# Performance work log

Hardware: AMD Instinct MI355X
Metric: run time of the kernel (lower is better)

The kernel has to match this reference:

```python
import jax, jax.numpy as jnp
import numpy as np

N = 50000
E = 200000
IN = 165
HID = 100
H1, H2, H3 = 8, 8, 1
NC = 2
DIM1 = HID * H1  # 800
DIM2 = HID * H2  # 800
NEG_SLOPE = 0.2


def setup_inputs() -> dict:
    key = jax.random.key(0)
    ks = jax.random.split(key, 20)
    p = lambda k, shape: jax.random.normal(k, shape, jnp.float32) * 0.05
    x = jax.random.normal(ks[0], (N, IN), jnp.float32)
    edge_index = jax.random.randint(ks[1], (2, E), 0, N, jnp.int64)
    return {
        "x": x,
        "edge_index": edge_index,
        "W1": p(ks[2], (IN, H1 * HID)), "a1s": p(ks[3], (H1, HID)),
        "a1d": p(ks[4], (H1, HID)), "b1": jnp.zeros((H1 * HID,), jnp.float32),
        "W2": p(ks[5], (DIM1, H2 * HID)), "a2s": p(ks[6], (H2, HID)),
        "a2d": p(ks[7], (H2, HID)), "b2": jnp.zeros((H2 * HID,), jnp.float32),
        # gat3: 800 -> 2, 1 head, mean (concat=False)
        "W3": p(ks[8], (DIM2, H3 * NC)), "a3s": p(ks[9], (H3, NC)),
        "a3d": p(ks[10], (H3, NC)), "b3": jnp.zeros((NC,), jnp.float32),
        # residual / skip linears (bias=False), stored [in, out]
        "Wres1": p(ks[11], (DIM1, DIM2)),
        "Wres2": p(ks[12], (DIM2, NC)),
        "Wskip": p(ks[13], (IN, NC)),
    }


def gat_conv(x, W, a_src, a_dst, b, src, dst, n, heads, ch, concat):
    # h: [n, heads, ch] projected node features
    h = (x @ W).reshape(n, heads, ch)
    e_src = (h * a_src).sum(-1)  # [n, heads]
    e_dst = (h * a_dst).sum(-1)
    # per-edge attention logits, LeakyReLU as in PyG GATConv
    e = jax.nn.leaky_relu(e_src[src] + e_dst[dst], NEG_SLOPE)  # [Etot, heads]
    # segment softmax over incoming edges of each destination node
    m = jax.ops.segment_max(e, dst, num_segments=n)
    ex = jnp.exp(e - m[dst])
    denom = jax.ops.segment_sum(ex, dst, num_segments=n)
    alpha = ex / (denom[dst] + 1e-16)
    # weighted scatter-aggregation of source messages
    out = jax.ops.segment_sum(alpha[:, :, None] * h[src], dst, num_segments=n)
    out = out.reshape(n, heads * ch) if concat else out.mean(axis=1)
    return out + b


def reference(x, edge_index, W1, a1s, a1d, b1, W2, a2s, a2d, b2,
              W3, a3s, a3d, b3, Wres1, Wres2, Wskip):
    n = x.shape[0]
    loop = jnp.arange(n, dtype=edge_index.dtype)  # PyG adds self-loops by default
    src = jnp.concatenate([edge_index[0], loop])
    dst = jnp.concatenate([edge_index[1], loop])

    h1 = jax.nn.elu(gat_conv(x, W1, a1s, a1d, b1, src, dst, n, H1, HID, True))
    h2 = gat_conv(h1, W2, a2s, a2d, b2, src, dst, n, H2, HID, True) + h1 @ Wres1
    h2 = jax.nn.elu(h2)
    logits = gat_conv(h2, W3, a3s, a3d, b3, src, dst, n, H3, NC, False)
    logits = logits + h2 @ Wres2 + x @ Wskip
    return logits
```

## Files before the change

kernel.cpp:

```cpp
#include <hip/hip_runtime.h>

#define NN     50000
#define NE     200000
#define ETOT   250000
#define FIN    165
#define KP1    192
#define HEADS  8
#define CH     100
#define DIM    800
#define MPAD   50048
#define NP1    896
#define DIM2   1600
#define NP2    1664
#define NEG    0.2f
#define CHK    64

typedef unsigned short u16;
typedef unsigned int   u32;
typedef __bf16 bf16x8 __attribute__((ext_vector_type(8)));
typedef float  f32x4  __attribute__((ext_vector_type(4)));

__device__ __forceinline__ u16 f2b(float f) {
  u32 u = __float_as_uint(f);
  u = (u + 0x7FFFu + ((u >> 16) & 1u)) >> 16;
  return (u16)u;
}
__device__ __forceinline__ float b2f(u16 u) { return __uint_as_float(((u32)u) << 16); }

__global__ void k_count(const int* __restrict__ ei, int* __restrict__ cnt) {
  int e = blockIdx.x * 256 + threadIdx.x;
  if (e >= ETOT) return;
  int d = (e < NE) ? ei[NE + e] : (e - NE);
  atomicAdd(&cnt[d], 1);
}
__global__ void k_bsum(const int* __restrict__ cnt, int* __restrict__ bs) {
  __shared__ int sm[256];
  int i = blockIdx.x * 256 + threadIdx.x;
  sm[threadIdx.x] = (i < NN) ? cnt[i] : 0;
  __syncthreads();
  for (int off = 128; off; off >>= 1) {
    if (threadIdx.x < off) sm[threadIdx.x] += sm[threadIdx.x + off];
    __syncthreads();
  }
  if (!threadIdx.x) bs[blockIdx.x] = sm[0];
}
__global__ void k_top(int* __restrict__ bs, int* __restrict__ rs, int nb) {
  __shared__ int sm[256];
  int t = threadIdx.x;
  int v = (t < nb) ? bs[t] : 0;
  sm[t] = v; __syncthreads();
  for (int off = 1; off < 256; off <<= 1) {
    int add = (t >= off) ? sm[t - off] : 0;
    __syncthreads();
    sm[t] += add;
    __syncthreads();
  }
  if (t < nb) bs[t] = sm[t] - v;
  if (!t) rs[NN] = ETOT;
}
__global__ void k_scan(const int* __restrict__ cnt, const int* __restrict__ bs, int* __restrict__ rs) {
  __shared__ int sm[256];
  int t = threadIdx.x, i = blockIdx.x * 256 + t;
  int v = (i < NN) ? cnt[i] : 0;
  sm[t] = v; __syncthreads();
  for (int off = 1; off < 256; off <<= 1) {
    int add = (t >= off) ? sm[t - off] : 0;
    __syncthreads();
    sm[t] += add;
    __syncthreads();
  }
  if (i < NN) rs[i] = bs[blockIdx.x] + sm[t] - v;
}
__global__ void k_fill(const int* __restrict__ ei, const int* __restrict__ rs,
                       int* __restrict__ cur, int* __restrict__ esrc) {
  int e = blockIdx.x * 256 + threadIdx.x;
  if (e >= ETOT) return;
  int s, d;
  if (e < NE) { s = ei[e]; d = ei[NE + e]; } else { s = d = e - NE; }
  int pos = atomicAdd(&cur[d], 1);
  esrc[rs[d] + pos] = s;
}

__global__ void k_cvt_x(const float* __restrict__ x, u16* __restrict__ A) {
  int idx = blockIdx.x * 256 + threadIdx.x;
  int r = idx / KP1, k = idx - r * KP1;
  float v = (r < NN && k < FIN) ? x[r * FIN + k] : 0.f;
  A[idx] = f2b(v);
}
__global__ void k_cvt_w1(const float* __restrict__ W1, u16* __restrict__ Bt) {
  int idx = blockIdx.x * 256 + threadIdx.x;
  int j = idx / KP1, k = idx - j * KP1;
  float v = (j < DIM && k < FIN) ? W1[k * DIM + j] : 0.f;
  Bt[idx] = f2b(v);
}
__global__ void k_cvt_w2(const float* __restrict__ W2, const float* __restrict__ Wr1,
                         u16* __restrict__ Bt) {
  int idx = blockIdx.x * 256 + threadIdx.x;
  int j = idx / DIM, k = idx - j * DIM;
  float v = 0.f;
  if (j < DIM) v = W2[k * DIM + j];
  else if (j < 2 * DIM) v = Wr1[k * DIM + (j - DIM)];
  Bt[idx] = f2b(v);
}
__global__ void k_wa(const float* __restrict__ W, const float* __restrict__ as,
                     const float* __restrict__ ad, u16* __restrict__ Wt,
                     int Kin, int Kpad, int Dsp) {
  int idx = blockIdx.x * 256 + threadIdx.x;
  if (idx >= 16 * Kpad) return;
  int j = idx / Kpad, k = idx - j * Kpad;
  int h = j & 7;
  const float* a = ((j < 8) ? as : ad) + h * CH;
  float s = 0.f;
  if (k < Kin) {
    const float* wr = W + (size_t)k * DIM + h * CH;
    for (int c = 0; c < CH; ++c) s += wr[c] * a[c];
  }
  Wt[(size_t)(Dsp + j) * Kpad + k] = f2b(s);
}

__device__ __forceinline__ void gl_lds16(const u16* g, u16* l) {
  __builtin_amdgcn_global_load_lds((const __attribute__((address_space(1))) void*)g,
                                   (__attribute__((address_space(3))) void*)l, 16, 0, 0);
}

__global__ __launch_bounds__(256) void k_gemm(const u16* __restrict__ A, const u16* __restrict__ Bt,
                                              u16* __restrict__ C, float* __restrict__ es,
                                              float* __restrict__ ed, int ksteps, int K,
                                              int Dsplit, int Nreal, int ldC) {
  __shared__ __align__(16) u16 lA[2][128 * 32];
  __shared__ __align__(16) u16 lB[2][128 * 32];
  int t = threadIdx.x;
  int lane = t & 63, wv = t >> 6;

  int nwg = gridDim.x * gridDim.y;
  int h = blockIdx.y * gridDim.x + blockIdx.x;
  int q = nwg >> 3, r8 = nwg & 7;
  int xcd = h & 7, i8 = h >> 3;
  int ln = (xcd < r8 ? xcd * (q + 1) : r8 * (q + 1) + (xcd - r8) * q) + i8;
  int tn = (ln % gridDim.x) * 128, tm = (ln / gridDim.x) * 128;

  int wr = (wv >> 1) * 64, wc = (wv & 1) * 64;
  int rl = lane & 15, kl = (lane >> 4) * 8;
  int srow = t >> 2, scb = (t & 3) * 8;

  f32x4 acc[4][4];
#pragma unroll
  for (int i = 0; i < 4; ++i)
#pragma unroll
    for (int j = 0; j < 4; ++j) acc[i][j] = (f32x4){0.f, 0.f, 0.f, 0.f};

  auto stage = [&](int buf, int ks) {
    int k0 = ks * 32;
#pragma unroll
    for (int r = 0; r < 2; ++r) {
      int row = srow + r * 64;
      int chunk = (r * 256 + t) * 8;
      gl_lds16(A + (size_t)(tm + row) * K + k0 + scb, &lA[buf][chunk]);
      gl_lds16(Bt + (size_t)(tn + row) * K + k0 + scb, &lB[buf][chunk]);
    }
  };

  stage(0, 0);
  int cur = 0;
  for (int ks = 0; ks < ksteps; ++ks) {
    __syncthreads();
    if (ks + 1 < ksteps) stage(cur ^ 1, ks + 1);
    bf16x8 af[4], bfr[4];
#pragma unroll
    for (int i = 0; i < 4; ++i) {
      af[i]  = *(const bf16x8*)&lA[cur][(wr + i * 16 + rl) * 32 + kl];
      bfr[i] = *(const bf16x8*)&lB[cur][(wc + i * 16 + rl) * 32 + kl];
    }
#pragma unroll
    for (int i = 0; i < 4; ++i)
#pragma unroll
      for (int j = 0; j < 4; ++j)
        acc[i][j] = __builtin_amdgcn_mfma_f32_16x16x32_bf16(af[i], bfr[j], acc[i][j], 0, 0, 0);
    cur ^= 1;
  }
  int rq = (lane >> 4) * 4;
#pragma unroll
  for (int i = 0; i < 4; ++i) {
#pragma unroll
    for (int j = 0; j < 4; ++j) {
      int col = tn + wc + j * 16 + rl;
      if (col < Dsplit) {
#pragma unroll
        for (int q2 = 0; q2 < 4; ++q2) {
          int row = tm + wr + i * 16 + rq + q2;
          C[(size_t)row * ldC + col] = f2b(acc[i][j][q2]);
        }
      } else if (col < Nreal) {
        int cj = col - Dsplit;
        float* dst = (cj < 8) ? es : ed;
        int hh = cj & 7;
#pragma unroll
        for (int q2 = 0; q2 < 4; ++q2) {
          int row = tm + wr + i * 16 + rq + q2;
          dst[(size_t)row * 8 + hh] = acc[i][j][q2];
        }
      }
    }
  }
}


__global__ __launch_bounds__(256) void k_agg1(const int* __restrict__ rs, const int* __restrict__ esrc,
    const u16* __restrict__ Hp, const float* __restrict__ es, const float* __restrict__ ed,
    const float* __restrict__ bias, u16* __restrict__ out) {
  __shared__ float sm_ex[CHK * 8];
  __shared__ float sm_den[8];
  __shared__ int   sm_src[CHK];
  int n = blockIdx.x, t = threadIdx.x;
  if (t < 8) sm_den[t] = 0.f;
  int beg = rs[n], end = rs[n + 1];
  int c = t * 4;
  int h = t / 25;
  float edv = (t < 200) ? 0.f : 0.f;
  float a0 = 0.f, a1 = 0.f, a2 = 0.f, a3 = 0.f;
  __syncthreads();
  for (int ch = beg; ch < end; ch += CHK) {
    int ce = min(end, ch + CHK);
    int m = ce - ch;
    if (t < m) sm_src[t] = esrc[ch + t];
    __syncthreads();
    for (int i = t; i < m * 8; i += 256) {
      int e8 = i >> 3, hh = i & 7;
      float xv = es[sm_src[e8] * 8 + hh] + ed[n * 8 + hh];
      xv = xv > 0.f ? xv : NEG * xv;
      float e = __expf(xv);
      sm_ex[i] = e;
      atomicAdd(&sm_den[hh], e);
    }
    __syncthreads();
    if (t < 200) {
      for (int j = 0; j < m; ++j) {
        float w = sm_ex[j * 8 + h];
        ushort4 u = *(const ushort4*)(Hp + (size_t)sm_src[j] * DIM + c);
        a0 += w * b2f(u.x); a1 += w * b2f(u.y); a2 += w * b2f(u.z); a3 += w * b2f(u.w);
      }
    }
    __syncthreads();
  }
  if (t >= 200) return;
  float inv = 1.f / (sm_den[h] + 1e-16f);
  const float4 bb = *(const float4*)(bias + c);
  float v0 = a0 * inv + bb.x, v1 = a1 * inv + bb.y, v2 = a2 * inv + bb.z, v3 = a3 * inv + bb.w;
  v0 = v0 > 0.f ? v0 : __expf(v0) - 1.f;
  v1 = v1 > 0.f ? v1 : __expf(v1) - 1.f;
  v2 = v2 > 0.f ? v2 : __expf(v2) - 1.f;
  v3 = v3 > 0.f ? v3 : __expf(v3) - 1.f;
  ushort4 o;
  o.x = f2b(v0); o.y = f2b(v1); o.z = f2b(v2); o.w = f2b(v3);
  *(ushort4*)(out + (size_t)n * DIM + c) = o;
  (void)edv;
}

__global__ __launch_bounds__(256) void k_agg2f(const int* __restrict__ rs, const int* __restrict__ esrc,
    const u16* __restrict__ Hp, const float* __restrict__ es, const float* __restrict__ ed,
    const float* __restrict__ bias, const u16* __restrict__ resid,
    const float* __restrict__ W3, const float* __restrict__ Wres2,
    const float* __restrict__ a3s, const float* __restrict__ a3d, const float* __restrict__ b3,
    const float* __restrict__ skp,
    float* __restrict__ H3p, float* __restrict__ base,
    float* __restrict__ es3, float* __restrict__ ed3) {
  __shared__ float sm_ex[CHK * 8];
  __shared__ float sm_den[8];
  __shared__ int   sm_src[CHK];
  __shared__ float red[4][4];
  int n = blockIdx.x, t = threadIdx.x;
  int lane = t & 63, wv = t >> 6;
  if (t < 8) sm_den[t] = 0.f;
  int beg = rs[n], end = rs[n + 1];
  int c = t * 4;
  int h = t / 25;
  float a0 = 0.f, a1 = 0.f, a2 = 0.f, a3 = 0.f;
  __syncthreads();
  for (int ch = beg; ch < end; ch += CHK) {
    int ce = min(end, ch + CHK);
    int m = ce - ch;
    if (t < m) sm_src[t] = esrc[ch + t];
    __syncthreads();
    for (int i = t; i < m * 8; i += 256) {
      int e8 = i >> 3, hh = i & 7;
      float xv = es[sm_src[e8] * 8 + hh] + ed[n * 8 + hh];
      xv = xv > 0.f ? xv : NEG * xv;
      float e = __expf(xv);
      sm_ex[i] = e;
      atomicAdd(&sm_den[hh], e);
    }
    __syncthreads();
    if (t < 200) {
      for (int j = 0; j < m; ++j) {
        float w = sm_ex[j * 8 + h];
        ushort4 u = *(const ushort4*)(Hp + (size_t)sm_src[j] * DIM2 + c);
        a0 += w * b2f(u.x); a1 += w * b2f(u.y); a2 += w * b2f(u.z); a3 += w * b2f(u.w);
      }
    }
    __syncthreads();
  }
  float p0 = 0.f, p1 = 0.f, r0 = 0.f, r1 = 0.f;
  if (t < 200) {
    float inv = 1.f / (sm_den[h] + 1e-16f);
    const float4 bb = *(const float4*)(bias + c);
    ushort4 rr = *(const ushort4*)(resid + (size_t)n * DIM2 + c);
    float v0 = a0 * inv + bb.x + b2f(rr.x);
    float v1 = a1 * inv + bb.y + b2f(rr.y);
    float v2 = a2 * inv + bb.z + b2f(rr.z);
    float v3 = a3 * inv + bb.w + b2f(rr.w);
    v0 = v0 > 0.f ? v0 : __expf(v0) - 1.f;
    v1 = v1 > 0.f ? v1 : __expf(v1) - 1.f;
    v2 = v2 > 0.f ? v2 : __expf(v2) - 1.f;
    v3 = v3 > 0.f ? v3 : __expf(v3) - 1.f;
    const float4 w3a = *(const float4*)(W3 + 2 * c);
    const float4 w3b = *(const float4*)(W3 + 2 * c + 4);
    const float4 wra = *(const float4*)(Wres2 + 2 * c);
    const float4 wrb = *(const float4*)(Wres2 + 2 * c + 4);
    p0 = v0 * w3a.x + v1 * w3a.z + v2 * w3b.x + v3 * w3b.z;
    p1 = v0 * w3a.y + v1 * w3a.w + v2 * w3b.y + v3 * w3b.w;
    r0 = v0 * wra.x + v1 * wra.z + v2 * wrb.x + v3 * wrb.z;
    r1 = v0 * wra.y + v1 * wra.w + v2 * wrb.y + v3 * wrb.w;
  }
#pragma unroll
  for (int off = 32; off; off >>= 1) {
    p0 += __shfl_down(p0, off); p1 += __shfl_down(p1, off);
    r0 += __shfl_down(r0, off); r1 += __shfl_down(r1, off);
  }
  if (!lane) { red[wv][0] = p0; red[wv][1] = p1; red[wv][2] = r0; red[wv][3] = r1; }
  __syncthreads();
  if (!t) {
    float P0 = red[0][0] + red[1][0] + red[2][0] + red[3][0];
    float P1 = red[0][1] + red[1][1] + red[2][1] + red[3][1];
    float R0 = red[0][2] + red[1][2] + red[2][2] + red[3][2];
    float R1 = red[0][3] + red[1][3] + red[2][3] + red[3][3];
    H3p[2 * n] = P0; H3p[2 * n + 1] = P1;
    es3[n] = P0 * a3s[0] + P1 * a3s[1];
    ed3[n] = P0 * a3d[0] + P1 * a3d[1];
    base[2 * n]     = R0 + skp[2 * n]     + b3[0];
    base[2 * n + 1] = R1 + skp[2 * n + 1] + b3[1];
  }
}

__global__ __launch_bounds__(256) void k_l3x(const float* __restrict__ x,
    const float* __restrict__ Wskip, float* __restrict__ skp) {
  int wv = threadIdx.x >> 6, lane = threadIdx.x & 63;
  int n = blockIdx.x * 4 + wv;
  if (n >= NN) return;
  float s0 = 0.f, s1 = 0.f;
  const float* xr = x + (size_t)n * FIN;
  for (int c = lane; c < FIN; c += 64) {
    float v = xr[c];
    s0 += v * Wskip[2 * c]; s1 += v * Wskip[2 * c + 1];
  }
#pragma unroll
  for (int off = 32; off; off >>= 1) {
    s0 += __shfl_down(s0, off); s1 += __shfl_down(s1, off);
  }
  if (!lane) { skp[2 * n] = s0; skp[2 * n + 1] = s1; }
}

__global__ void k_l3agg(const int* __restrict__ rs, const int* __restrict__ esrc,
                        const float* __restrict__ H3p, const float* __restrict__ base,
                        const float* __restrict__ es3, const float* __restrict__ ed3,
                        float* __restrict__ out) {
  int n = blockIdx.x * 256 + threadIdx.x;
  if (n >= NN) return;
  int beg = rs[n], end = rs[n + 1];
  float edv = ed3[n];
  float den = 0.f, a0 = 0.f, a1 = 0.f;
  for (int j = beg; j < end; ++j) {
    int s = esrc[j];
    float e = es3[s] + edv;
    e = e > 0.f ? e : NEG * e;
    float exv = __expf(e);
    den += exv;
    a0 += exv * H3p[2 * s];
    a1 += exv * H3p[2 * s + 1];
  }
  float inv = 1.f / (den + 1e-16f);
  out[2 * n]     = base[2 * n]     + a0 * inv;
  out[2 * n + 1] = base[2 * n + 1] + a1 * inv;
}

extern "C" void kernel_launch(void* const* d_in, const int* in_sizes, int n_in,
                              void* d_out, int out_size, void* d_ws, size_t ws_size,
                              hipStream_t stream) {
  (void)in_sizes; (void)n_in; (void)out_size; (void)ws_size;
  const float* x    = (const float*)d_in[0];
  const int*   ei   = (const int*)d_in[1];
  const float* W1   = (const float*)d_in[2];
  const float* a1s  = (const float*)d_in[3];
  const float* a1d  = (const float*)d_in[4];
  const float* b1   = (const float*)d_in[5];
  const float* W2   = (const float*)d_in[6];
  const float* a2s  = (const float*)d_in[7];
  const float* a2d  = (const float*)d_in[8];
  const float* b2   = (const float*)d_in[9];
  const float* W3   = (const float*)d_in[10];
  const float* a3s  = (const float*)d_in[11];
  const float* a3d  = (const float*)d_in[12];
  const float* b3   = (const float*)d_in[13];
  const float* Wr1  = (const float*)d_in[14];
  const float* Wr2  = (const float*)d_in[15];
  const float* Wsk  = (const float*)d_in[16];
  float* out = (float*)d_out;

  char* w = (char*)d_ws;
  size_t off = 0;
  auto alloc = [&](size_t bytes) { void* p = w + off; off += (bytes + 255) & ~(size_t)255; return p; };
  int* cnt   = (int*)alloc((size_t)NN * 4);
  int* cur   = (int*)alloc((size_t)NN * 4);
  int* rs    = (int*)alloc((size_t)(NN + 1) * 4);
  int* bs    = (int*)alloc(256 * 4);
  int* esrc  = (int*)alloc((size_t)ETOT * 4);
  float* es  = (float*)alloc((size_t)MPAD * HEADS * 4);
  float* ed  = (float*)alloc((size_t)MPAD * HEADS * 4);
  u16* W1t   = (u16*)alloc((size_t)NP1 * KP1 * 2);
  u16* W2t   = (u16*)alloc((size_t)NP2 * DIM * 2);
  float* H3p = (float*)alloc((size_t)NN * 2 * 4);
  float* base= (float*)alloc((size_t)NN * 2 * 4);
  float* es3 = (float*)alloc((size_t)NN * 4);
  float* ed3 = (float*)alloc((size_t)NN * 4);
  float* skp = (float*)alloc((size_t)NN * 2 * 4);
  u16* bufB  = (u16*)alloc((size_t)MPAD * DIM * 2);
  u16* bufA  = (u16*)alloc((size_t)MPAD * DIM2 * 2);
  u16* H1p   = bufA;
  u16* G2    = bufA;
  u16* A1    = bufA + (size_t)MPAD * DIM;

  const int nb = (NN + 255) / 256;
  const int ge = (ETOT + 255) / 256;

  hipMemsetAsync(cnt, 0, (size_t)NN * 4, stream);
  hipMemsetAsync(cur, 0, (size_t)NN * 4, stream);
  k_count<<<ge, 256, 0, stream>>>(ei, cnt);
  k_bsum <<<nb, 256, 0, stream>>>(cnt, bs);
  k_top  <<<1, 256, 0, stream>>>(bs, rs, nb);
  k_scan <<<nb, 256, 0, stream>>>(cnt, bs, rs);
  k_fill <<<ge, 256, 0, stream>>>(ei, rs, cur, esrc);

  k_cvt_x <<<(MPAD * KP1) / 256, 256, 0, stream>>>(x, A1);
  k_cvt_w1<<<(NP1 * KP1) / 256, 256, 0, stream>>>(W1, W1t);
  k_wa    <<<(16 * KP1 + 255) / 256, 256, 0, stream>>>(W1, a1s, a1d, W1t, FIN, KP1, DIM);
  k_cvt_w2<<<(NP2 * DIM) / 256, 256, 0, stream>>>(W2, Wr1, W2t);
  k_wa    <<<(16 * DIM + 255) / 256, 256, 0, stream>>>(W2, a2s, a2d, W2t, DIM, DIM, DIM2);
  k_l3x   <<<(NN + 3) / 4, 256, 0, stream>>>(x, Wsk, skp);

  k_gemm<<<dim3(NP1 / 128, MPAD / 128), 256, 0, stream>>>(A1, W1t, H1p, es, ed,
                                                          KP1 / 32, KP1, DIM, DIM + 16, DIM);
  k_agg1<<<NN, 256, 0, stream>>>(rs, esrc, H1p, es, ed, b1, bufB);

  k_gemm<<<dim3(NP2 / 128, MPAD / 128), 256, 0, stream>>>(bufB, W2t, G2, es, ed,
                                                          DIM / 32, DIM, DIM2, DIM2 + 16, DIM2);
  k_agg2f<<<NN, 256, 0, stream>>>(rs, esrc, G2, es, ed, b2, G2 + DIM,
                                  W3, Wr2, a3s, a3d, b3, skp, H3p, base, es3, ed3);

  k_l3agg<<<nb, 256, 0, stream>>>(rs, esrc, H3p, base, es3, ed3, out);
}
```

Measured before the change: 508.2 us.

## Fuse prep kernels into one launch and swizzle GEMM LDS layout

Merges the input/weight conversion, attention-weight folding, skip projection and counter zeroing into a single block-partitioned prep kernel, replacing six launches and two memsets. It also changes the GEMM's LDS staging to a 16-row-grouped, XOR-swizzled layout so the MFMA fragment reads avoid bank conflicts. The fused kernel adds branch dispatch per block, and the swizzle must match exactly between the global-to-LDS writes and the fragment reads.

```diff
diff --git a/kernel.cpp b/kernel.cpp
--- a/kernel.cpp
+++ b/kernel.cpp
@@ -81,32 +81,16 @@
   esrc[rs[d] + pos] = s;
 }
 
-__global__ void k_cvt_x(const float* __restrict__ x, u16* __restrict__ A) {
-  int idx = blockIdx.x * 256 + threadIdx.x;
-  int r = idx / KP1, k = idx - r * KP1;
-  float v = (r < NN && k < FIN) ? x[r * FIN + k] : 0.f;
-  A[idx] = f2b(v);
-}
-__global__ void k_cvt_w1(const float* __restrict__ W1, u16* __restrict__ Bt) {
-  int idx = blockIdx.x * 256 + threadIdx.x;
-  int j = idx / KP1, k = idx - j * KP1;
-  float v = (j < DIM && k < FIN) ? W1[k * DIM + j] : 0.f;
-  Bt[idx] = f2b(v);
-}
-__global__ void k_cvt_w2(const float* __restrict__ W2, const float* __restrict__ Wr1,
-                         u16* __restrict__ Bt) {
-  int idx = blockIdx.x * 256 + threadIdx.x;
-  int j = idx / DIM, k = idx - j * DIM;
-  float v = 0.f;
-  if (j < DIM) v = W2[k * DIM + j];
-  else if (j < 2 * DIM) v = Wr1[k * DIM + (j - DIM)];
-  Bt[idx] = f2b(v);
-}
-__global__ void k_wa(const float* __restrict__ W, const float* __restrict__ as,
-                     const float* __restrict__ ad, u16* __restrict__ Wt,
-                     int Kin, int Kpad, int Dsp) {
-  int idx = blockIdx.x * 256 + threadIdx.x;
-  if (idx >= 16 * Kpad) return;
+#define PR_X   37536
+#define PR_W1  38208
+#define PR_WA1 38220
+#define PR_W2  43420
+#define PR_WA2 43470
+#define PR_L3X 55970
+#define PR_Z   56361
+
+__device__ __forceinline__ void d_wa(int idx, const float* W, const float* as,
+                                     const float* ad, u16* Wt, int Kin, int Kpad, int Dsp) {
   int j = idx / Kpad, k = idx - j * Kpad;
   int h = j & 7;
   const float* a = ((j < 8) ? as : ad) + h * CH;
@@ -116,6 +100,59 @@
     for (int c = 0; c < CH; ++c) s += wr[c] * a[c];
   }
   Wt[(size_t)(Dsp + j) * Kpad + k] = f2b(s);
+}
+
+__global__ __launch_bounds__(256) void k_prep(const float* __restrict__ x,
+    const float* __restrict__ W1, const float* __restrict__ a1s, const float* __restrict__ a1d,
+    const float* __restrict__ W2, const float* __restrict__ Wr1,
+    const float* __restrict__ a2s, const float* __restrict__ a2d,
+    const float* __restrict__ Wsk,
+    u16* __restrict__ A1, u16* __restrict__ W1t, u16* __restrict__ W2t,
+    float* __restrict__ skp, int* __restrict__ cnt, int* __restrict__ cur) {
+  int b = blockIdx.x, t = threadIdx.x;
+  if (b < PR_X) {
+    int idx = b * 256 + t;
+    int r = idx / KP1, k = idx - r * KP1;
+    float v = (r < NN && k < FIN) ? x[r * FIN + k] : 0.f;
+    A1[idx] = f2b(v);
+  } else if (b < PR_W1) {
+    int idx = (b - PR_X) * 256 + t;
+    int j = idx / KP1, k = idx - j * KP1;
+    float v = (j < DIM && k < FIN) ? W1[k * DIM + j] : 0.f;
+    W1t[idx] = f2b(v);
+  } else if (b < PR_WA1) {
+    int idx = (b - PR_W1) * 256 + t;
+    d_wa(idx, W1, a1s, a1d, W1t, FIN, KP1, DIM);
+  } else if (b < PR_W2) {
+    int idx = (b - PR_WA1) * 256 + t;
+    int j = idx / DIM, k = idx - j * DIM;
+    float v = 0.f;
+    if (j < DIM) v = W2[k * DIM + j];
+    else if (j < 2 * DIM) v = Wr1[k * DIM + (j - DIM)];
+    W2t[idx] = f2b(v);
+  } else if (b < PR_WA2) {
+    int idx = (b - PR_W2) * 256 + t;
+    d_wa(idx, W2, a2s, a2d, W2t, DIM, DIM, DIM2);
+  } else if (b < PR_L3X) {
+    int wv = t >> 6, lane = t & 63;
+    int n = (b - PR_WA2) * 4 + wv;
+    if (n >= NN) return;
+    float s0 = 0.f, s1 = 0.f;
+    const float* xr = x + (size_t)n * FIN;
+    for (int c = lane; c < FIN; c += 64) {
+      float v = xr[c];
+      s0 += v * Wsk[2 * c]; s1 += v * Wsk[2 * c + 1];
+    }
+#pragma unroll
+    for (int off = 32; off; off >>= 1) {
+      s0 += __shfl_down(s0, off); s1 += __shfl_down(s1, off);
+    }
+    if (!lane) { skp[2 * n] = s0; skp[2 * n + 1] = s1; }
+  } else {
+    int i = (b - PR_L3X) * 256 + t;
+    if (i < NN) cnt[i] = 0;
+    else if (i < 2 * NN) cur[i - NN] = 0;
+  }
 }
 
 __device__ __forceinline__ void gl_lds16(const u16* g, u16* l) {
@@ -141,7 +178,7 @@
 
   int wr = (wv >> 1) * 64, wc = (wv & 1) * 64;
   int rl = lane & 15, kl = (lane >> 4) * 8;
-  int srow = t >> 2, scb = (t & 3) * 8;
+  int rdo = rl * 32 + (kl ^ (((rl >> 3) & 1) << 4));
 
   f32x4 acc[4][4];
 #pragma unroll
@@ -153,10 +190,11 @@
     int k0 = ks * 32;
 #pragma unroll
     for (int r = 0; r < 2; ++r) {
-      int row = srow + r * 64;
-      int chunk = (r * 256 + t) * 8;
-      gl_lds16(A + (size_t)(tm + row) * K + k0 + scb, &lA[buf][chunk]);
-      gl_lds16(Bt + (size_t)(tn + row) * K + k0 + scb, &lB[buf][chunk]);
+      int chunk = r * 256 + t;
+      int row = ((chunk >> 6) << 4) + ((chunk >> 2) & 15);
+      int kb  = ((chunk & 3) << 3) ^ (((chunk >> 5) & 1) << 4);
+      gl_lds16(A + (size_t)(tm + row) * K + k0 + kb, &lA[buf][chunk * 8]);
+      gl_lds16(Bt + (size_t)(tn + row) * K + k0 + kb, &lB[buf][chunk * 8]);
     }
   };
 
@@ -168,8 +206,8 @@
     bf16x8 af[4], bfr[4];
 #pragma unroll
     for (int i = 0; i < 4; ++i) {
-      af[i]  = *(const bf16x8*)&lA[cur][(wr + i * 16 + rl) * 32 + kl];
-      bfr[i] = *(const bf16x8*)&lB[cur][(wc + i * 16 + rl) * 32 + kl];
+      af[i]  = *(const bf16x8*)&lA[cur][(((wr + i * 16) >> 4) << 9) + rdo];
+      bfr[i] = *(const bf16x8*)&lB[cur][(((wc + i * 16) >> 4) << 9) + rdo];
     }
 #pragma unroll
     for (int i = 0; i < 4; ++i)
@@ -216,7 +254,6 @@
   int beg = rs[n], end = rs[n + 1];
   int c = t * 4;
   int h = t / 25;
-  float edv = (t < 200) ? 0.f : 0.f;
   float a0 = 0.f, a1 = 0.f, a2 = 0.f, a3 = 0.f;
   __syncthreads();
   for (int ch = beg; ch < end; ch += CHK) {
@@ -253,7 +290,6 @@
   ushort4 o;
   o.x = f2b(v0); o.y = f2b(v1); o.z = f2b(v2); o.w = f2b(v3);
   *(ushort4*)(out + (size_t)n * DIM + c) = o;
-  (void)edv;
 }
 
 __global__ __launch_bounds__(256) void k_agg2f(const int* __restrict__ rs, const int* __restrict__ esrc,
@@ -341,24 +377,6 @@
   }
 }
 
-__global__ __launch_bounds__(256) void k_l3x(const float* __restrict__ x,
-    const float* __restrict__ Wskip, float* __restrict__ skp) {
-  int wv = threadIdx.x >> 6, lane = threadIdx.x & 63;
-  int n = blockIdx.x * 4 + wv;
-  if (n >= NN) return;
-  float s0 = 0.f, s1 = 0.f;
-  const float* xr = x + (size_t)n * FIN;
-  for (int c = lane; c < FIN; c += 64) {
-    float v = xr[c];
-    s0 += v * Wskip[2 * c]; s1 += v * Wskip[2 * c + 1];
-  }
-#pragma unroll
-  for (int off = 32; off; off >>= 1) {
-    s0 += __shfl_down(s0, off); s1 += __shfl_down(s1, off);
-  }
-  if (!lane) { skp[2 * n] = s0; skp[2 * n + 1] = s1; }
-}
-
 __global__ void k_l3agg(const int* __restrict__ rs, const int* __restrict__ esrc,
                         const float* __restrict__ H3p, const float* __restrict__ base,
                         const float* __restrict__ es3, const float* __restrict__ ed3,
@@ -431,21 +449,15 @@
   const int nb = (NN + 255) / 256;
   const int ge = (ETOT + 255) / 256;
 
-  hipMemsetAsync(cnt, 0, (size_t)NN * 4, stream);
-  hipMemsetAsync(cur, 0, (size_t)NN * 4, stream);
+  k_prep<<<PR_Z, 256, 0, stream>>>(x, W1, a1s, a1d, W2, Wr1, a2s, a2d, Wsk,
+                                   A1, W1t, W2t, skp, cnt, cur);
+
   k_count<<<ge, 256, 0, stream>>>(ei, cnt);
   k_bsum <<<nb, 256, 0, stream>>>(cnt, bs);
   k_top  <<<1, 256, 0, stream>>>(bs, rs, nb);
   k_scan <<<nb, 256, 0, stream>>>(cnt, bs, rs);
   k_fill <<<ge, 256, 0, stream>>>(ei, rs, cur, esrc);
 
-  k_cvt_x <<<(MPAD * KP1) / 256, 256, 0, stream>>>(x, A1);
-  k_cvt_w1<<<(NP1 * KP1) / 256, 256, 0, stream>>>(W1, W1t);
-  k_wa    <<<(16 * KP1 + 255) / 256, 256, 0, stream>>>(W1, a1s, a1d, W1t, FIN, KP1, DIM);
-  k_cvt_w2<<<(NP2 * DIM) / 256, 256, 0, stream>>>(W2, Wr1, W2t);
-  k_wa    <<<(16 * DIM + 255) / 256, 256, 0, stream>>>(W2, a2s, a2d, W2t, DIM, DIM, DIM2);
-  k_l3x   <<<(NN + 3) / 4, 256, 0, stream>>>(x, Wsk, skp);
-
   k_gemm<<<dim3(NP1 / 128, MPAD / 128), 256, 0, stream>>>(A1, W1t, H1p, es, ed,
                                                           KP1 / 32, KP1, DIM, DIM + 16, DIM);
   k_agg1<<<NN, 256, 0, stream>>>(rs, esrc, H1p, es, ed, b1, bufB);
```

New measurement: 480.9 us. 1.06x faster.
